# Optimization experiments

Hardware: AMD Instinct MI355X
Metric: run time of the kernel (lower is better)

The kernel has to match this reference:

```python
import jax, jax.numpy as jnp
import numpy as np

NUM_HEADS = 16

def rotate_half(x):
    h = x.shape[-1] // 2
    return jnp.concatenate([-x[..., h:], x[..., :h]], axis=-1)

def setup_inputs() -> dict:
    key = jax.random.key(0)
    k1, k2, k3 = jax.random.split(key, 3)
    B, S, H = 2, 2048, 1024
    x = jax.random.normal(k1, (B, S, H), dtype=jnp.float32)
    W_qkv = jax.random.normal(k2, (3 * H, H), dtype=jnp.float32) * (1.0 / np.sqrt(H))
    W_proj = jax.random.normal(k3, (H, H), dtype=jnp.float32) * (1.0 / np.sqrt(H))
    return {"x": x, "W_qkv": W_qkv, "W_proj": W_proj}

def reference(x, W_qkv, W_proj):
    B, S, H = x.shape
    nH = NUM_HEADS
    hd = H // nH
    # QKV projection (bias=False): y = x @ W.T
    qkv = jnp.einsum('bsh,oh->bso', x, W_qkv)  # [B,S,3H]
    q, k, v = jnp.split(qkv, 3, axis=-1)
    def to_heads(t):
        return t.reshape(B, S, nH, hd).transpose(0, 2, 1, 3)  # [B,nH,S,hd]
    q, k, v = to_heads(q), to_heads(k), to_heads(v)
    # RoPE on first half of head_dim; freqs dim = hd//2
    half = hd // 2
    inv_freq = 1.0 / (10000.0 ** (jnp.arange(0, hd, 2, dtype=jnp.float32) / hd))  # [hd//2]
    t = jnp.arange(S, dtype=jnp.float32)
    freqs = t[:, None] * inv_freq[None, :]  # [S, hd//2]
    cos = jnp.cos(freqs)[None, None]  # [1,1,S,hd//2]
    sin = jnp.sin(freqs)[None, None]
    q_half, q_rest = q[..., :half], q[..., half:]
    k_half, k_rest = k[..., :half], k[..., half:]
    q_rot = q_half * cos + rotate_half(q_half) * sin
    k_rot = k_half * cos + rotate_half(k_half) * sin
    q = jnp.concatenate([q_rot, q_rest], axis=-1)
    k = jnp.concatenate([k_rot, k_rest], axis=-1)
    # scaled dot-product attention (no mask, dropout=0 / eval)
    scale = 1.0 / np.sqrt(hd)
    att = jnp.einsum('bhqd,bhkd->bhqk', q, k) * scale  # [B,nH,S,S]
    att = jax.nn.softmax(att, axis=-1)
    out = jnp.einsum('bhqk,bhkd->bhqd', att, v)  # [B,nH,S,hd]
    out = out.transpose(0, 2, 1, 3).reshape(B, S, H)
    return jnp.einsum('bsh,oh->bso', out, W_proj)
```

## Files before the change

kernel.cpp:

```cpp
#include <hip/hip_runtime.h>
#include <math.h>

#define SEQ  2048
#define NHD  16
#define HD   64
#define HDIM 1024

typedef short s16x8 __attribute__((ext_vector_type(8)));
typedef short s16x4 __attribute__((ext_vector_type(4)));
typedef float f32x4 __attribute__((ext_vector_type(4)));

typedef const __attribute__((address_space(1))) unsigned int* gp_t;
typedef __attribute__((address_space(3))) unsigned int* lp_t;

__device__ __forceinline__ void async16(const short* g, short* l) {
    __builtin_amdgcn_global_load_lds((gp_t)g, (lp_t)l, 16, 0, 0);
}

__device__ __forceinline__ short f2bf(float f) {
    unsigned int u = __float_as_uint(f);
    u += 0x7fff + ((u >> 16) & 1);
    return (short)(u >> 16);
}
__device__ __forceinline__ float bf2f(short s) {
    return __uint_as_float(((unsigned int)(unsigned short)s) << 16);
}

__global__ void detect_k(const unsigned short* __restrict__ x, int* __restrict__ flag) {
    int cnt = 0;
    #pragma unroll 4
    for (int j = 0; j < 32; ++j) {
        unsigned short h = x[threadIdx.x * 32 + j];
        int e = (h >> 7) & 0xFF;
        cnt += (e >= 100 && e <= 140) ? 1 : 0;
    }
    __shared__ int tot;
    if (threadIdx.x == 0) tot = 0;
    __syncthreads();
    atomicAdd(&tot, cnt);
    __syncthreads();
    if (threadIdx.x == 0) *flag = (tot > (8192 * 9) / 10) ? 1 : 0;
}

#define XG4  (4096 * 1024 / 4)
#define WQG4 (3072 * 1024 / 4)
#define WPG4 (1024 * 1024 / 4)
__global__ void cvt_all_k(const void* __restrict__ xr, const void* __restrict__ wqr,
                          const void* __restrict__ wpr, short* __restrict__ xo,
                          short* __restrict__ wqo, short* __restrict__ wpo,
                          const int* __restrict__ flag) {
    int i = blockIdx.x * 256 + threadIdx.x;
    const void* in; short* out; int j;
    if (i < XG4)             { in = xr;  out = xo;  j = i; }
    else if (i < XG4 + WQG4) { in = wqr; out = wqo; j = i - XG4; }
    else                     { in = wpr; out = wpo; j = i - XG4 - WQG4; }
    if (*flag) {
        ((s16x4*)out)[j] = ((const s16x4*)in)[j];
    } else {
        f32x4 v = ((const f32x4*)in)[j];
        s16x4 r;
        r[0] = f2bf(v[0]); r[1] = f2bf(v[1]);
        r[2] = f2bf(v[2]); r[3] = f2bf(v[3]);
        ((s16x4*)out)[j] = r;
    }
}

__global__ void rope_tab_k(float2* __restrict__ tab) {
    int i = blockIdx.x * 256 + threadIdx.x;
    if (i >= SEQ * 32) return;
    int s = i >> 5, d = i & 31;
    float invf = (float)pow(10000.0, -(double)d / 32.0);
    float af = (float)s * invf;
    double a = (double)af;
    tab[i] = make_float2((float)cos(a), (float)sin(a));
}

template<int MODE>
__global__ __launch_bounds__(256, 2)
void gemm_bt(const short* __restrict__ A, const short* __restrict__ B,
             short* __restrict__ q, short* __restrict__ kbuf, short* __restrict__ vt,
             float* __restrict__ C, const float2* __restrict__ tab,
             int K, int N) {
    __shared__ __align__(16) short As[128 * 32];
    __shared__ __align__(16) short Bs[128 * 32];
    const int tid  = threadIdx.x;
    const int w    = tid >> 6, lane = tid & 63;
    const int quad = lane >> 4, l16 = lane & 15;
    const int wm = (w >> 1) * 64, wn = (w & 1) * 64;
    const int rowA0 = blockIdx.y * 128;
    const int colB0 = blockIdx.x * 128;

    f32x4 acc[4][4] = {};

    for (int kb = 0; kb < K; kb += 32) {
        __syncthreads();
        #pragma unroll
        for (int i = 0; i < 2; ++i) {
            int cidx = i * 256 + w * 64 + lane;
            int row = cidx >> 2, sc = cidx & 3;
            int c = sc ^ (row & 3);
            async16(&A[(long)(rowA0 + row) * K + kb + c * 8],
                    &As[(i * 256 + w * 64) * 8]);
            async16(&B[(long)(colB0 + row) * K + kb + c * 8],
                    &Bs[(i * 256 + w * 64) * 8]);
        }
        __syncthreads();

        s16x8 af[4], bfr[4];
        const int slot = quad ^ (l16 & 3);
        #pragma unroll
        for (int mi = 0; mi < 4; ++mi)
            af[mi] = *(const s16x8*)&As[(wm + mi * 16 + l16) * 32 + slot * 8];
        #pragma unroll
        for (int ni = 0; ni < 4; ++ni)
            bfr[ni] = *(const s16x8*)&Bs[(wn + ni * 16 + l16) * 32 + slot * 8];
        #pragma unroll
        for (int mi = 0; mi < 4; ++mi)
            #pragma unroll
            for (int ni = 0; ni < 4; ++ni)
                acc[mi][ni] = __builtin_amdgcn_mfma_f32_16x16x32_bf16(
                    af[mi], bfr[ni], acc[mi][ni], 0, 0, 0);
    }

    const int cb = colB0 + wn;
    if (MODE == 1) {
        #pragma unroll
        for (int mi = 0; mi < 4; ++mi) {
            #pragma unroll
            for (int r = 0; r < 4; ++r) {
                int gm = rowA0 + wm + mi * 16 + quad * 4 + r;
                float* cp = C + (long)gm * N + cb + l16;
                #pragma unroll
                for (int ni = 0; ni < 4; ++ni)
                    cp[ni * 16] = acc[mi][ni][r];
            }
        }
        return;
    }
    const int sector = cb >> 10;
    const int head   = (cb & 1023) >> 6;
    if (sector < 2) {
        const float sc = (sector == 0) ? 0.18033688f : 1.0f;
        __syncthreads();
        short* arena = (w < 2) ? (As + w * 2048) : (Bs + (w - 2) * 2048);
        const int gmb = rowA0 + wm;
        const int b = gmb >> 11, s0 = gmb & 2047;
        short* dst0 = (sector == 0 ? q : kbuf)
                    + ((long)((b * NHD + head) * SEQ + s0)) * HD;
        #pragma unroll
        for (int hh = 0; hh < 2; ++hh) {
            #pragma unroll
            for (int m2 = 0; m2 < 2; ++m2) {
                int mi = hh * 2 + m2;
                #pragma unroll
                for (int r = 0; r < 4; ++r) {
                    int lrow = m2 * 16 + quad * 4 + r;
                    int s = s0 + hh * 32 + lrow;
                    float v0 = acc[mi][0][r], v1 = acc[mi][1][r];
                    float v2 = acc[mi][2][r], v3 = acc[mi][3][r];
                    float2 cs0 = tab[s * 32 + l16];
                    float2 cs1 = tab[s * 32 + 16 + l16];
                    float n0 = v0 * cs0.x - v1 * cs0.y;
                    float n1 = v1 * cs1.x + v0 * cs1.y;
                    arena[lrow * 64 + l16]      = f2bf(n0 * sc);
                    arena[lrow * 64 + l16 + 16] = f2bf(n1 * sc);
                    arena[lrow * 64 + l16 + 32] = f2bf(v2 * sc);
                    arena[lrow * 64 + l16 + 48] = f2bf(v3 * sc);
                }
            }
            #pragma unroll
            for (int it = 0; it < 4; ++it) {
                int chunk = it * 64 + lane;
                int row = chunk >> 3, cc = chunk & 7;
                s16x8 vv = *(const s16x8*)&arena[row * 64 + cc * 8];
                *(s16x8*)&dst0[(hh * 32 + row) * HD + cc * 8] = vv;
            }
        }
    } else {
        #pragma unroll
        for (int mi = 0; mi < 4; ++mi) {
            int srow = rowA0 + wm + mi * 16 + quad * 4;
            int b = srow >> 11, s0 = srow & 2047;
            #pragma unroll
            for (int ni = 0; ni < 4; ++ni) {
                s16x4 pk;
                #pragma unroll
                for (int r = 0; r < 4; ++r) pk[r] = f2bf(acc[mi][ni][r]);
                *(s16x4*)&vt[((long)((b * NHD + head) * HD + ni * 16 + l16)) * SEQ + s0] = pk;
            }
        }
    }
}

__global__ __launch_bounds__(256, 4)
void flash_attn(const short* __restrict__ Q, const short* __restrict__ K,
                const short* __restrict__ Vt, short* __restrict__ opart,
                float* __restrict__ lpart, int nt) {
    __shared__ __align__(16) short Ks[64 * 64];
    __shared__ __align__(16) short Vs[64 * 64];
    const int tid  = threadIdx.x;
    const int w    = tid >> 6, lane = tid & 63;
    const int quad = lane >> 4, l16 = lane & 15;
    const int bh = blockIdx.y;
    const int qb = blockIdx.x * 128;
    const int z  = blockIdx.z;
    const short* Qp = Q  + (long)bh * SEQ * HD + (long)qb * HD;
    const short* Kp = K  + (long)bh * SEQ * HD;
    const short* Vp = Vt + (long)bh * HD * SEQ;

    s16x8 aq[2][2];
    #pragma unroll
    for (int mi = 0; mi < 2; ++mi)
        #pragma unroll
        for (int ks = 0; ks < 2; ++ks)
            aq[mi][ks] = *(const s16x8*)&Qp[(w * 32 + mi * 16 + l16) * HD
                                            + ks * 32 + quad * 8];

    s16x8 ones8;
    #pragma unroll
    for (int j = 0; j < 8; ++j) ones8[j] = (short)0x3F80;

    f32x4 oacc[2][4] = {};
    f32x4 lacc[2] = {};

    for (int kt = z * nt; kt < z * nt + nt; ++kt) {
        __syncthreads();
        #pragma unroll
        for (int i = 0; i < 2; ++i) {
            int cidx = i * 256 + w * 64 + lane;
            int row = cidx >> 3, sc = cidx & 7;
            int c = sc ^ (row & 7);
            async16(&Kp[(kt * 64 + row) * HD + c * 8], &Ks[(i * 256 + w * 64) * 8]);
            async16(&Vp[(long)row * SEQ + kt * 64 + c * 8], &Vs[(i * 256 + w * 64) * 8]);
        }
        __syncthreads();

        f32x4 st[2][4] = {};
        #pragma unroll
        for (int ki = 0; ki < 4; ++ki) {
            s16x8 ak0 = *(const s16x8*)&Ks[(ki * 16 + l16) * 64 + (quad ^ (l16 & 7)) * 8];
            s16x8 ak1 = *(const s16x8*)&Ks[(ki * 16 + l16) * 64 + ((4 + quad) ^ (l16 & 7)) * 8];
            #pragma unroll
            for (int mi = 0; mi < 2; ++mi) {
                st[mi][ki] = __builtin_amdgcn_mfma_f32_16x16x32_bf16(
                    ak0, aq[mi][0], st[mi][ki], 0, 0, 0);
                st[mi][ki] = __builtin_amdgcn_mfma_f32_16x16x32_bf16(
                    ak1, aq[mi][1], st[mi][ki], 0, 0, 0);
            }
        }

        s16x8 bp[2][2];
        #pragma unroll
        for (int mi = 0; mi < 2; ++mi)
            #pragma unroll
            for (int t = 0; t < 2; ++t) {
                s16x8 f;
                #pragma unroll
                for (int r = 0; r < 4; ++r) {
                    f[r]     = f2bf(exp2f(st[mi][2 * t][r]));
                    f[4 + r] = f2bf(exp2f(st[mi][2 * t + 1][r]));
                }
                bp[mi][t] = f;
            }

        #pragma unroll
        for (int t = 0; t < 2; ++t) {
            #pragma unroll
            for (int nd = 0; nd < 4; ++nd) {
                int d = nd * 16 + l16;
                s16x4 va = *(const s16x4*)&Vs[d * 64
                             + ((4 * t + (quad >> 1)) ^ (l16 & 7)) * 8
                             + (quad & 1) * 4];
                s16x4 vb = *(const s16x4*)&Vs[d * 64
                             + ((4 * t + 2 + (quad >> 1)) ^ (l16 & 7)) * 8
                             + (quad & 1) * 4];
                s16x8 av = {va[0], va[1], va[2], va[3],
                            vb[0], vb[1], vb[2], vb[3]};
                #pragma unroll
                for (int mi = 0; mi < 2; ++mi)
                    oacc[mi][nd] = __builtin_amdgcn_mfma_f32_16x16x32_bf16(
                        av, bp[mi][t], oacc[mi][nd], 0, 0, 0);
            }
            #pragma unroll
            for (int mi = 0; mi < 2; ++mi)
                lacc[mi] = __builtin_amdgcn_mfma_f32_16x16x32_bf16(
                    ones8, bp[mi][t], lacc[mi], 0, 0, 0);
        }
    }

    #pragma unroll
    for (int mi = 0; mi < 2; ++mi) {
        int srow = qb + w * 32 + mi * 16 + l16;
        long prow = (long)(z * 2 * NHD + bh) * SEQ + srow;
        if (quad == 0) lpart[prow] = lacc[mi][0];
        short* op = opart + prow * 64 + quad * 4;
        #pragma unroll
        for (int nd = 0; nd < 4; ++nd) {
            s16x4 pk;
            #pragma unroll
            for (int r = 0; r < 4; ++r) pk[r] = f2bf(oacc[mi][nd][r]);
            *(s16x4*)&op[nd * 16] = pk;
        }
    }
}

__global__ __launch_bounds__(256)
void merge_k(const short* __restrict__ opart, const float* __restrict__ lpart,
             short* __restrict__ att) {
    int idx = blockIdx.x * 256 + threadIdx.x;
    int t16 = idx & 15, rowg = idx >> 4;
    int bh = rowg >> 11, srow = rowg & 2047;
    float inv = 1.0f / (lpart[rowg] + lpart[65536 + rowg]);
    s16x4 o1 = *(const s16x4*)&opart[(long)rowg * 64 + t16 * 4];
    s16x4 o2 = *(const s16x4*)&opart[(long)(65536 + rowg) * 64 + t16 * 4];
    int b = bh >> 4, h = bh & 15;
    short* dst = att + ((long)(b * SEQ + srow)) * HDIM + h * HD + t16 * 4;
    s16x4 r;
    #pragma unroll
    for (int j = 0; j < 4; ++j)
        r[j] = f2bf((bf2f(o1[j]) + bf2f(o2[j])) * inv);
    *(s16x4*)dst = r;
}

extern "C" void kernel_launch(void* const* d_in, const int* in_sizes, int n_in,
                              void* d_out, int out_size, void* d_ws, size_t ws_size,
                              hipStream_t stream) {
    const void* x_raw  = d_in[0];
    const void* Wq_raw = d_in[1];
    const void* Wp_raw = d_in[2];
    for (int i = 0; i < n_in; ++i) {
        if      (in_sizes[i] == 4096 * 1024) x_raw  = d_in[i];
        else if (in_sizes[i] == 3072 * 1024) Wq_raw = d_in[i];
        else if (in_sizes[i] == 1024 * 1024) Wp_raw = d_in[i];
    }
    float* out = (float*)d_out;

    const size_t MB = 1u << 20;
    char* ws = (char*)d_ws;
    short*  q     = (short*)(ws);
    short*  k     = (short*)(ws +  8 * MB);
    short*  vt    = (short*)(ws + 16 * MB);
    short*  xbf   = (short*)(ws + 24 * MB);
    short*  att   = xbf;
    short*  wqkv  = (short*)(ws + 32 * MB);
    short*  wprj  = (short*)(ws + 38 * MB);
    float2* tab   = (float2*)(ws + 40 * MB);
    int*    flag  = (int*)(ws + 40 * MB + 512 * 1024);
    short*  opart = (short*)(ws + 41 * MB);
    float*  lprt  = (float*)(ws + 57 * MB);

    detect_k<<<dim3(1), dim3(256), 0, stream>>>((const unsigned short*)x_raw, flag);

    cvt_all_k<<<dim3((XG4 + WQG4 + WPG4) / 256), dim3(256), 0, stream>>>(
        x_raw, Wq_raw, Wp_raw, xbf, wqkv, wprj, flag);

    rope_tab_k<<<dim3(SEQ * 32 / 256), dim3(256), 0, stream>>>(tab);

    gemm_bt<0><<<dim3(3072 / 128, 4096 / 128), dim3(256), 0, stream>>>(
        xbf, wqkv, q, k, vt, (float*)nullptr, tab, 1024, 3072);

    flash_attn<<<dim3(SEQ / 128, 2 * NHD, 2), dim3(256), 0, stream>>>(
        q, k, vt, opart, lprt, 16);

    merge_k<<<dim3(65536 * 16 / 256), dim3(256), 0, stream>>>(opart, lprt, att);

    gemm_bt<1><<<dim3(1024 / 128, 4096 / 128), dim3(256), 0, stream>>>(
        att, wprj, (short*)nullptr, (short*)nullptr, (short*)nullptr, out, tab, 1024, 1024);
}
```

Before: 220.1 us.

## Double-buffer LDS tiles in GEMM and attention kernels, reorder attention grid

```diff
diff --git a/kernel.cpp b/kernel.cpp
--- a/kernel.cpp
+++ b/kernel.cpp
@@ -81,8 +81,8 @@
              short* __restrict__ q, short* __restrict__ kbuf, short* __restrict__ vt,
              float* __restrict__ C, const float2* __restrict__ tab,
              int K, int N) {
-    __shared__ __align__(16) short As[128 * 32];
-    __shared__ __align__(16) short Bs[128 * 32];
+    __shared__ __align__(16) short As[2][128 * 32];
+    __shared__ __align__(16) short Bs[2][128 * 32];
     const int tid  = threadIdx.x;
     const int w    = tid >> 6, lane = tid & 63;
     const int quad = lane >> 4, l16 = lane & 15;
@@ -90,30 +90,35 @@
     const int rowA0 = blockIdx.y * 128;
     const int colB0 = blockIdx.x * 128;
 
-    f32x4 acc[4][4] = {};
-
-    for (int kb = 0; kb < K; kb += 32) {
-        __syncthreads();
+    auto stage = [&](int buf, int kb) {
         #pragma unroll
         for (int i = 0; i < 2; ++i) {
             int cidx = i * 256 + w * 64 + lane;
             int row = cidx >> 2, sc = cidx & 3;
             int c = sc ^ (row & 3);
             async16(&A[(long)(rowA0 + row) * K + kb + c * 8],
-                    &As[(i * 256 + w * 64) * 8]);
+                    &As[buf][(i * 256 + w * 64) * 8]);
             async16(&B[(long)(colB0 + row) * K + kb + c * 8],
-                    &Bs[(i * 256 + w * 64) * 8]);
-        }
+                    &Bs[buf][(i * 256 + w * 64) * 8]);
+        }
+    };
+
+    f32x4 acc[4][4] = {};
+    stage(0, 0);
+
+    for (int kb = 0, it = 0; kb < K; kb += 32, ++it) {
+        const int cur = it & 1;
         __syncthreads();
+        if (kb + 32 < K) stage(cur ^ 1, kb + 32);
 
         s16x8 af[4], bfr[4];
         const int slot = quad ^ (l16 & 3);
         #pragma unroll
         for (int mi = 0; mi < 4; ++mi)
-            af[mi] = *(const s16x8*)&As[(wm + mi * 16 + l16) * 32 + slot * 8];
+            af[mi] = *(const s16x8*)&As[cur][(wm + mi * 16 + l16) * 32 + slot * 8];
         #pragma unroll
         for (int ni = 0; ni < 4; ++ni)
-            bfr[ni] = *(const s16x8*)&Bs[(wn + ni * 16 + l16) * 32 + slot * 8];
+            bfr[ni] = *(const s16x8*)&Bs[cur][(wn + ni * 16 + l16) * 32 + slot * 8];
         #pragma unroll
         for (int mi = 0; mi < 4; ++mi)
             #pragma unroll
@@ -142,7 +147,7 @@
     if (sector < 2) {
         const float sc = (sector == 0) ? 0.18033688f : 1.0f;
         __syncthreads();
-        short* arena = (w < 2) ? (As + w * 2048) : (Bs + (w - 2) * 2048);
+        short* arena = (w < 2) ? (&As[0][0] + w * 2048) : (&Bs[0][0] + (w - 2) * 2048);
         const int gmb = rowA0 + wm;
         const int b = gmb >> 11, s0 = gmb & 2047;
         short* dst0 = (sector == 0 ? q : kbuf)
@@ -196,50 +201,58 @@
 void flash_attn(const short* __restrict__ Q, const short* __restrict__ K,
                 const short* __restrict__ Vt, short* __restrict__ opart,
                 float* __restrict__ lpart, int nt) {
-    __shared__ __align__(16) short Ks[64 * 64];
-    __shared__ __align__(16) short Vs[64 * 64];
+    __shared__ __align__(16) short Ks[2][64 * 64];
+    __shared__ __align__(16) short Vs[2][64 * 64];
     const int tid  = threadIdx.x;
     const int w    = tid >> 6, lane = tid & 63;
     const int quad = lane >> 4, l16 = lane & 15;
-    const int bh = blockIdx.y;
-    const int qb = blockIdx.x * 128;
-    const int z  = blockIdx.z;
+    const int bh = blockIdx.x >> 1;
+    const int z  = blockIdx.x & 1;
+    const int qb = blockIdx.y * 128;
     const short* Qp = Q  + (long)bh * SEQ * HD + (long)qb * HD;
     const short* Kp = K  + (long)bh * SEQ * HD;
     const short* Vp = Vt + (long)bh * HD * SEQ;
-
-    s16x8 aq[2][2];
-    #pragma unroll
-    for (int mi = 0; mi < 2; ++mi)
-        #pragma unroll
-        for (int ks = 0; ks < 2; ++ks)
-            aq[mi][ks] = *(const s16x8*)&Qp[(w * 32 + mi * 16 + l16) * HD
-                                            + ks * 32 + quad * 8];
-
-    s16x8 ones8;
-    #pragma unroll
-    for (int j = 0; j < 8; ++j) ones8[j] = (short)0x3F80;
-
-    f32x4 oacc[2][4] = {};
-    f32x4 lacc[2] = {};
-
-    for (int kt = z * nt; kt < z * nt + nt; ++kt) {
-        __syncthreads();
+    const int kt0 = z * nt;
+
+    auto stage = [&](int buf, int kt) {
         #pragma unroll
         for (int i = 0; i < 2; ++i) {
             int cidx = i * 256 + w * 64 + lane;
             int row = cidx >> 3, sc = cidx & 7;
             int c = sc ^ (row & 7);
-            async16(&Kp[(kt * 64 + row) * HD + c * 8], &Ks[(i * 256 + w * 64) * 8]);
-            async16(&Vp[(long)row * SEQ + kt * 64 + c * 8], &Vs[(i * 256 + w * 64) * 8]);
-        }
+            async16(&Kp[(kt * 64 + row) * HD + c * 8],
+                    &Ks[buf][(i * 256 + w * 64) * 8]);
+            async16(&Vp[(long)row * SEQ + kt * 64 + c * 8],
+                    &Vs[buf][(i * 256 + w * 64) * 8]);
+        }
+    };
+
+    s16x8 aq[2][2];
+    #pragma unroll
+    for (int mi = 0; mi < 2; ++mi)
+        #pragma unroll
+        for (int ks = 0; ks < 2; ++ks)
+            aq[mi][ks] = *(const s16x8*)&Qp[(w * 32 + mi * 16 + l16) * HD
+                                            + ks * 32 + quad * 8];
+
+    s16x8 ones8;
+    #pragma unroll
+    for (int j = 0; j < 8; ++j) ones8[j] = (short)0x3F80;
+
+    f32x4 oacc[2][4] = {};
+    f32x4 lacc[2] = {};
+
+    stage(0, kt0);
+    for (int it = 0; it < nt; ++it) {
+        const int cur = it & 1;
         __syncthreads();
+        if (it + 1 < nt) stage(cur ^ 1, kt0 + it + 1);
 
         f32x4 st[2][4] = {};
         #pragma unroll
         for (int ki = 0; ki < 4; ++ki) {
-            s16x8 ak0 = *(const s16x8*)&Ks[(ki * 16 + l16) * 64 + (quad ^ (l16 & 7)) * 8];
-            s16x8 ak1 = *(const s16x8*)&Ks[(ki * 16 + l16) * 64 + ((4 + quad) ^ (l16 & 7)) * 8];
+            s16x8 ak0 = *(const s16x8*)&Ks[cur][(ki * 16 + l16) * 64 + (quad ^ (l16 & 7)) * 8];
+            s16x8 ak1 = *(const s16x8*)&Ks[cur][(ki * 16 + l16) * 64 + ((4 + quad) ^ (l16 & 7)) * 8];
             #pragma unroll
             for (int mi = 0; mi < 2; ++mi) {
                 st[mi][ki] = __builtin_amdgcn_mfma_f32_16x16x32_bf16(
@@ -268,10 +281,10 @@
             #pragma unroll
             for (int nd = 0; nd < 4; ++nd) {
                 int d = nd * 16 + l16;
-                s16x4 va = *(const s16x4*)&Vs[d * 64
+                s16x4 va = *(const s16x4*)&Vs[cur][d * 64
                              + ((4 * t + (quad >> 1)) ^ (l16 & 7)) * 8
                              + (quad & 1) * 4];
-                s16x4 vb = *(const s16x4*)&Vs[d * 64
+                s16x4 vb = *(const s16x4*)&Vs[cur][d * 64
                              + ((4 * t + 2 + (quad >> 1)) ^ (l16 & 7)) * 8
                              + (quad & 1) * 4];
                 s16x8 av = {va[0], va[1], va[2], va[3],
@@ -359,7 +372,7 @@
     gemm_bt<0><<<dim3(3072 / 128, 4096 / 128), dim3(256), 0, stream>>>(
         xbf, wqkv, q, k, vt, (float*)nullptr, tab, 1024, 3072);
 
-    flash_attn<<<dim3(SEQ / 128, 2 * NHD, 2), dim3(256), 0, stream>>>(
+    flash_attn<<<dim3(2 * NHD * 2, SEQ / 128), dim3(256), 0, stream>>>(
         q, k, vt, opart, lprt, 16);
 
     merge_k<<<dim3(65536 * 16 / 256), dim3(256), 0, stream>>>(opart, lprt, att);
```

After: 209.7 us. -4.7%, faster.
